# Kernel tuning notes

Measured on AMD Instinct MI355X. Metric: run time of the kernel, lower is better.

## Reference

```python
import jax, jax.numpy as jnp
import numpy as np

B, S, D = 4, 2048, 512
H, DH = 8, 64          # heads, dim_head; inner_dim = H*DH = D
QN, QP = -128, 127     # signed 8-bit range (LSQ, all_positive=False)
UQP = 255              # unsigned 8-bit range for softmax output

# scale-vector layout (one learnable LSQ scale per quantizer, as in the module)
# 0:s_hs 1:s_a_q 2:s_w_q 3:s_a_k 4:s_w_k 5:s_a_v 6:s_w_v
# 7:s_qk_a 8:s_qk_b 9:s_softmax 10:s_av_a 11:s_av_b 12:s_a_out 13:s_w_out

def fq(x, s, qn=QN, qp=QP):
    """LSQ fake quantization: clamp(round(x/s), qn, qp) * s, STE on round."""
    v = jnp.clip(x / s, qn, qp)
    vq = v + jax.lax.stop_gradient(jnp.round(v) - v)
    return vq * s


def setup_inputs() -> dict:
    key = jax.random.key(0)
    ks = jax.random.split(key, 6)
    hs = jax.random.normal(ks[0], (B, S, D), dtype=jnp.float32)
    w_std = 0.02
    Wq = jax.random.normal(ks[1], (D, D), dtype=jnp.float32) * w_std
    Wk = jax.random.normal(ks[2], (D, D), dtype=jnp.float32) * w_std
    Wv = jax.random.normal(ks[3], (D, D), dtype=jnp.float32) * w_std
    Wo = jax.random.normal(ks[4], (D, D), dtype=jnp.float32) * w_std
    bo = jnp.zeros((D,), dtype=jnp.float32)
    scales = jnp.array([
        0.03,    # s_hs: hs ~ N(0,1), clip at ~4 sigma
        0.03, 0.001,   # to_q act / weight
        0.03, 0.001,   # to_k act / weight
        0.03, 0.001,   # to_v act / weight
        0.02, 0.02,    # mul_qk a/b
        1.0 / 255.0,   # softmax output (unsigned)
        1.0 / 255.0, 0.02,  # mul_av a/b
        0.01, 0.001,   # to_out act / weight
    ], dtype=jnp.float32)
    return {"hs": hs, "Wq": Wq, "Wk": Wk, "Wv": Wv, "Wo": Wo, "bo": bo,
            "scales": scales}


def reference(hs, Wq, Wk, Wv, Wo, bo, scales):
    sc = scales
    scale = DH ** (-0.5)
    # quan_hs_before_attn (encoder_hidden_states = hs in self-attention)
    hs_q = fq(hs, sc[0])
    # Linear_Quan: LSQ-quantized activation @ LSQ-quantized weight
    def qlin(x, W, sa, sw):
        return jnp.einsum('bsd,ed->bse', fq(x, sa), fq(W, sw))
    q = qlin(hs_q, Wq, sc[1], sc[2])
    k = qlin(hs_q, Wk, sc[3], sc[4])
    v = qlin(hs_q, Wv, sc[5], sc[6])
    # 'b s (h d) -> b h s d'
    q = q.reshape(B, S, H, DH).transpose(0, 2, 1, 3)
    k = k.reshape(B, S, H, DH).transpose(0, 2, 1, 3)
    v = v.reshape(B, S, H, DH).transpose(0, 2, 1, 3)
    # QuanMMHead(q, k^T): quantize both operands, then matmul
    attn = jnp.einsum('bhsd,bhtd->bhst', fq(q, sc[7]), fq(k, sc[8])) * scale
    # QuanSoftmax: softmax then unsigned 8-bit fake quant of probabilities
    attn = fq(jax.nn.softmax(attn, axis=-1), sc[9], 0, UQP)
    # QuanMMHead(attn, v)
    out = jnp.einsum('bhst,bhtd->bhsd', fq(attn, sc[10]), fq(v, sc[11]))
    # '(b h) s d -> b s (h d)'
    out = out.transpose(0, 2, 1, 3).reshape(B, S, H * DH)
    # to_out[0]: Linear_Quan with bias (dropout is identity in eval)
    out = jnp.einsum('bsd,ed->bse', fq(out, sc[12]), fq(Wo, sc[13])) + bo
    return out
```

## Files before the change

### kernel.cpp

```cpp
#include <hip/hip_runtime.h>

typedef _Float16 half8  __attribute__((ext_vector_type(8)));
typedef float    f32x4  __attribute__((ext_vector_type(4)));
typedef int      i32x4  __attribute__((ext_vector_type(4)));
typedef unsigned short ushort8 __attribute__((ext_vector_type(8)));
typedef signed char char8 __attribute__((ext_vector_type(8)));

__device__ __forceinline__ float clampf(float v, float lo, float hi){
    return fminf(fmaxf(v, lo), hi);
}
__device__ __forceinline__ float b2f(unsigned short u){
    unsigned int x = ((unsigned int)u) << 16;
    return __builtin_bit_cast(float, x);
}
__device__ __forceinline__ unsigned short f2b(float f){
    unsigned int u = __builtin_bit_cast(unsigned int, f);
    u += 0x7FFFu + ((u >> 16) & 1u);
    return (unsigned short)(u >> 16);
}
__device__ __forceinline__ float fexp2(float x){ return __builtin_amdgcn_exp2f(x); }

__device__ __forceinline__ void gld_lds16(const void* g, void* lds_uniform){
    __builtin_amdgcn_global_load_lds(
        (const __attribute__((address_space(1))) void*)g,
        (__attribute__((address_space(3))) void*)lds_uniform, 16, 0, 0);
}

#define BW_WALL 0u
#define BW_WO   786432u
#define BW_AQ   1048576u
#define BW_AK   (BW_AQ + 4194304u)
#define BW_AV   (BW_AK + 4194304u)
#define BW_Q    (BW_AV + 4194304u)
#define BW_K    (BW_Q  + 8388608u)
#define BW_VT   (BW_K  + 8388608u)
#define BW_O    (BW_VT + 8388608u)

__global__ __launch_bounds__(256) void k_quant(
    const unsigned short* __restrict__ hs,
    const unsigned short* __restrict__ Wq, const unsigned short* __restrict__ Wk,
    const unsigned short* __restrict__ Wv, const unsigned short* __restrict__ Wo,
    signed char* __restrict__ w_all, signed char* __restrict__ wo8,
    signed char* __restrict__ aq, signed char* __restrict__ ak,
    signed char* __restrict__ av,
    const unsigned short* __restrict__ scu)
{
    int blk = blockIdx.x;
    if (blk < 512){
        int gid  = blk * 256 + threadIdx.x;
        int idx8 = gid * 8;
        int which = idx8 >> 18;
        int rem   = idx8 & 262143;
        const unsigned short* W = (which==0)? Wq : (which==1)? Wk : (which==2)? Wv : Wo;
        float sw = b2f((which<3) ? scu[2 + 2*which] : scu[13]);
        ushort8 w = *(const ushort8*)(W + rem);
        char8 o;
        #pragma unroll
        for (int j=0;j<8;j++)
            o[j] = (signed char)rintf(clampf(b2f(w[j])/sw, -128.f, 127.f));
        signed char* dst = (which<3) ? (w_all + which*262144 + rem) : (wo8 + rem);
        *(char8*)dst = o;
    } else {
        int gid = (blk - 512) * 256 + threadIdx.x;
        int i8 = gid * 8;
        float s0 = b2f(scu[0]), s1 = b2f(scu[1]), s3 = b2f(scu[3]), s5 = b2f(scu[5]);
        ushort8 h = *(const ushort8*)(hs + i8);
        char8 q, k, v;
        #pragma unroll
        for (int j=0;j<8;j++){
            float h1 = rintf(clampf(b2f(h[j])/s0, -128.f, 127.f)) * s0;
            q[j] = (signed char)rintf(clampf(h1/s1, -128.f, 127.f));
            k[j] = (signed char)rintf(clampf(h1/s3, -128.f, 127.f));
            v[j] = (signed char)rintf(clampf(h1/s5, -128.f, 127.f));
        }
        *(char8*)(aq+i8) = q;
        *(char8*)(ak+i8) = k;
        *(char8*)(av+i8) = v;
    }
}

__global__ __launch_bounds__(256) void k_gemm_qkv(
    const signed char* __restrict__ aq, const signed char* __restrict__ ak,
    const signed char* __restrict__ av, const signed char* __restrict__ w_all,
    _Float16* __restrict__ q16, _Float16* __restrict__ k16, _Float16* __restrict__ vt16,
    const unsigned short* __restrict__ scu)
{
    __shared__ __align__(16) union SMem {
        struct { signed char At[128][64]; signed char Bt[64][64]; } ab;
        _Float16 Vt[64][132];
    } sm;
    int tid = threadIdx.x;
    int m0 = blockIdx.x*128, n0 = blockIdx.y*64;
    int proj = blockIdx.y >> 3;
    const signed char* Ag = (proj==0)? aq : (proj==1)? ak : av;
    int w = tid>>6, lane = tid&63, l15 = lane&15, quad = lane>>4;
    int wm = w>>1, wn = w&1;
    i32x4 z = {0,0,0,0};
    i32x4 acc[4][2];
    #pragma unroll
    for (int i=0;i<4;i++)
      #pragma unroll
      for (int j=0;j<2;j++) acc[i][j] = z;

    for (int k0=0; k0<512; k0+=64){
        #pragma unroll
        for (int it=0; it<2; it++){
            int idx = it*256 + tid;
            int row = idx>>2, col = (idx&3)*16;
            int ubase = (it*256 + w*64)*16;
            gld_lds16(Ag + (m0+row)*512 + k0 + col, &sm.ab.At[0][0] + ubase);
        }
        {
            int row = tid>>2, col = (tid&3)*16;
            int ubase = (w*64)*16;
            gld_lds16(w_all + (n0+row)*512 + k0 + col, &sm.ab.Bt[0][0] + ubase);
        }
        __syncthreads();
        i32x4 af[4], bf[2];
        #pragma unroll
        for (int mt=0; mt<4; mt++)
            af[mt] = *(const i32x4*)(&sm.ab.At[wm*64+mt*16+l15][quad*16]);
        #pragma unroll
        for (int nt=0; nt<2; nt++)
            bf[nt] = *(const i32x4*)(&sm.ab.Bt[wn*32+nt*16+l15][quad*16]);
        #pragma unroll
        for (int mt=0; mt<4; mt++)
          #pragma unroll
          for (int nt=0; nt<2; nt++)
            acc[mt][nt] = __builtin_amdgcn_mfma_i32_16x16x64_i8(af[mt], bf[nt], acc[mt][nt], 0,0,0);
        __syncthreads();
    }

    float ssc = b2f(scu[1+2*proj]) * b2f(scu[2+2*proj]);
    float qs  = b2f((proj==0)? scu[7] : (proj==1)? scu[8] : scu[11]);
    if (proj < 2){
        #pragma unroll
        for (int mt=0; mt<4; mt++){
          #pragma unroll
          for (int nt=0; nt<2; nt++){
            int n = n0 + wn*32 + nt*16 + l15;
            int nloc = n & 511;
            int h = nloc>>6, d = nloc&63;
            #pragma unroll
            for (int r=0;r<4;r++){
              int m = m0 + wm*64 + mt*16 + quad*4 + r;
              int b = m>>11, s = m&2047;
              int bh = b*8 + h;
              float val = (float)acc[mt][nt][r] * ssc;
              float qv = rintf(clampf(val/qs, -128.f, 127.f));
              if (proj==0) q16[(bh*2048 + s)*64 + d] = (_Float16)qv;
              else         k16[(bh*2048 + s)*64 + d] = (_Float16)qv;
            }
          }
        }
    } else {
        #pragma unroll
        for (int mt=0; mt<4; mt++){
          #pragma unroll
          for (int nt=0; nt<2; nt++){
            int nl = wn*32 + nt*16 + l15;
            #pragma unroll
            for (int r=0;r<4;r++){
              int ml = wm*64 + mt*16 + quad*4 + r;
              float val = (float)acc[mt][nt][r] * ssc;
              sm.Vt[nl][ml] = (_Float16)rintf(clampf(val/qs, -128.f, 127.f));
            }
          }
        }
        __syncthreads();
        int vrow = tid >> 2;
        int vcol = (tid & 3) * 32;
        int nloc2 = (n0 & 511) + vrow;
        int h2 = nloc2 >> 6, d2 = nloc2 & 63;
        int bh2 = (m0 >> 11)*8 + h2;
        int s2 = (m0 & 2047) + vcol;
        _Float16* dst = vt16 + (bh2*64 + d2)*2048 + s2;
        #pragma unroll
        for (int i=0;i<4;i++)
            *(half8*)(dst + i*8) = *(const half8*)(&sm.Vt[vrow][vcol + i*8]);
    }
}

__global__ __launch_bounds__(512, 4) void k_attn(
    const _Float16* __restrict__ q16, const _Float16* __restrict__ k16,
    const _Float16* __restrict__ vt16, signed char* __restrict__ o8,
    const unsigned short* __restrict__ scu)
{
    __shared__ __align__(16) _Float16 Kbuf[2][64][72];
    __shared__ __align__(16) _Float16 p16[8][16][72];
    int tid = threadIdx.x;
    int w = tid>>6, lane = tid&63, l15 = lane&15, quad = lane>>4;
    int bh = blockIdx.x;
    int q0 = blockIdx.y*128 + w*16;
    float s9 = b2f(scu[9]), s10 = b2f(scu[10]);
    float al2 = b2f(scu[7]) * b2f(scu[8]) * 0.125f * 1.44269504088896341f;

    f32x4 z = {0.f,0.f,0.f,0.f};
    const _Float16* qr = q16 + (bh*2048 + q0 + l15)*64;
    half8 aq0 = *(const half8*)(qr + quad*8);
    half8 aq1 = *(const half8*)(qr + 32 + quad*8);

    const _Float16* kg    = k16  + bh*131072;
    const _Float16* vbase = vt16 + bh*131072;
    int srow = tid>>3, scol = (tid&7)*8;

    half8 kst = *(const half8*)(kg + tid*8);

    float l[4] = {0.f, 0.f, 0.f, 0.f};
    float cmx[32];

    #pragma unroll
    for (int ch=0; ch<32; ch++){
        int buf = ch & 1;
        *(half8*)(&Kbuf[buf][srow][scol]) = kst;
        __syncthreads();
        if (ch < 31)
            kst = *(const half8*)(kg + (ch+1)*4096 + tid*8);
        f32x4 s[4];
        #pragma unroll
        for (int j=0;j<4;j++){
            half8 bk0 = *(const half8*)(&Kbuf[buf][j*16+l15][quad*8]);
            half8 bk1 = *(const half8*)(&Kbuf[buf][j*16+l15][32+quad*8]);
            f32x4 t = __builtin_amdgcn_mfma_f32_16x16x32_f16(aq0, bk0, z, 0,0,0);
            s[j]    = __builtin_amdgcn_mfma_f32_16x16x32_f16(aq1, bk1, t, 0,0,0);
        }
        float mj[4];
        #pragma unroll
        for (int j=0;j<4;j++){
            mj[j] = fmaxf(fmaxf(s[j][0], s[j][1]), fmaxf(s[j][2], s[j][3]));
            #pragma unroll
            for (int r=0;r<4;r++)
                l[r] += fexp2(s[j][r]*al2);
        }
        cmx[ch] = fmaxf(fmaxf(mj[0], mj[1]), fmaxf(mj[2], mj[3]));
    }

    #pragma unroll
    for (int r=0;r<4;r++){
        #pragma unroll
        for (int d=1; d<16; d<<=1)
            l[r] += __shfl_xor(l[r], d, 64);
    }
    float inv_s9 = 1.0f / s9;
    float r910   = s9 / s10;
    float lq9[4];
    #pragma unroll
    for (int r=0;r<4;r++) lq9[r] = log2f(inv_s9 / l[r]);
    float lml = fmaxf(fmaxf(lq9[0], lq9[1]), fmaxf(lq9[2], lq9[3]));
    unsigned int mask = 0u;
    #pragma unroll
    for (int ch=0; ch<32; ch++){
        if (__ballot(fmaf(cmx[ch], al2, lml) > -1.0001f)) mask |= (1u << ch);
    }

    f32x4 oacc[4];
    #pragma unroll
    for (int dt=0; dt<4; dt++) oacc[dt] = z;
    for (int ch=0; ch<32; ch++){
        if (!(mask & (1u << ch))) continue;
        const _Float16* kc = kg + ch*4096;
        f32x4 s[4];
        #pragma unroll
        for (int j=0;j<4;j++){
            const _Float16* kr = kc + (j*16+l15)*64;
            half8 bk0 = *(const half8*)(kr + quad*8);
            half8 bk1 = *(const half8*)(kr + 32 + quad*8);
            f32x4 t = __builtin_amdgcn_mfma_f32_16x16x32_f16(aq0, bk0, z, 0,0,0);
            s[j]    = __builtin_amdgcn_mfma_f32_16x16x32_f16(aq1, bk1, t, 0,0,0);
        }
        float rmax[4];
        #pragma unroll
        for (int r=0;r<4;r++)
            rmax[r] = fmaxf(fmaxf(s[0][r], s[1][r]), fmaxf(s[2][r], s[3][r]));
        float rb = fmaxf(fmaxf(fmaf(rmax[0], al2, lq9[0]), fmaf(rmax[1], al2, lq9[1])),
                         fmaxf(fmaf(rmax[2], al2, lq9[2]), fmaf(rmax[3], al2, lq9[3])));
        if (!__ballot(rb > -1.0001f)) continue;

        float av[4][4];
        float amax = 0.f;
        #pragma unroll
        for (int j=0;j<4;j++){
            #pragma unroll
            for (int r=0;r<4;r++){
                float p1i = rintf(fminf(fexp2(fmaf(s[j][r], al2, lq9[r])), 255.f));
                float a   = rintf(fminf(p1i*r910, 127.f));
                av[j][r] = a;
                amax = fmaxf(amax, a);
            }
        }
        if (__ballot(amax > 0.f)){
            #pragma unroll
            for (int j=0;j<4;j++)
                #pragma unroll
                for (int r=0;r<4;r++)
                    p16[w][quad*4+r][j*16+l15] = (_Float16)av[j][r];
            half8 ap0 = *(const half8*)(&p16[w][l15][quad*8]);
            half8 ap1 = *(const half8*)(&p16[w][l15][32+quad*8]);
            #pragma unroll
            for (int dt=0; dt<4; dt++){
                const _Float16* vr0 = vbase + (dt*16+l15)*2048 + ch*64;
                half8 b0 = *(const half8*)(vr0 + quad*8);
                half8 b1 = *(const half8*)(vr0 + 32 + quad*8);
                oacc[dt] = __builtin_amdgcn_mfma_f32_16x16x32_f16(ap0, b0, oacc[dt], 0,0,0);
                oacc[dt] = __builtin_amdgcn_mfma_f32_16x16x32_f16(ap1, b1, oacc[dt], 0,0,0);
            }
        }
    }

    float s1011 = b2f(scu[10]) * b2f(scu[11]);
    float s12   = b2f(scu[12]);
    int b = bh>>3, h = bh&7;
    #pragma unroll
    for (int dt=0; dt<4; dt++){
        #pragma unroll
        for (int r=0;r<4;r++){
            float o = oacc[dt][r] * s1011;
            signed char v = (signed char)rintf(clampf(o/s12, -128.f, 127.f));
            o8[(b*2048 + q0 + quad*4 + r)*512 + h*64 + dt*16 + l15] = v;
        }
    }
}

__global__ __launch_bounds__(256) void k_gemm_out(
    const signed char* __restrict__ o8, const signed char* __restrict__ wo8,
    const unsigned short* __restrict__ bo, unsigned short* __restrict__ out,
    const unsigned short* __restrict__ scu)
{
    __shared__ __align__(16) signed char At[64][64];
    __shared__ __align__(16) signed char Bt[64][64];
    int tid = threadIdx.x;
    int m0 = blockIdx.x*64, n0 = blockIdx.y*64;
    int w = tid>>6, lane = tid&63, l15 = lane&15, quad = lane>>4;
    int wm = w>>1, wn = w&1;
    i32x4 z = {0,0,0,0};
    i32x4 acc[2][2];
    #pragma unroll
    for (int i=0;i<2;i++)
      #pragma unroll
      for (int j=0;j<2;j++) acc[i][j] = z;

    for (int k0=0; k0<512; k0+=64){
        {
            int row = tid>>2, col = (tid&3)*16;
            int ubase = (w*64)*16;
            gld_lds16(o8  + (m0+row)*512 + k0 + col, &At[0][0] + ubase);
        }
        {
            int row = tid>>2, col = (tid&3)*16;
            int ubase = (w*64)*16;
            gld_lds16(wo8 + (n0+row)*512 + k0 + col, &Bt[0][0] + ubase);
        }
        __syncthreads();
        i32x4 af[2], bf[2];
        #pragma unroll
        for (int mt=0; mt<2; mt++)
            af[mt] = *(const i32x4*)(&At[wm*32+mt*16+l15][quad*16]);
        #pragma unroll
        for (int nt=0; nt<2; nt++)
            bf[nt] = *(const i32x4*)(&Bt[wn*32+nt*16+l15][quad*16]);
        #pragma unroll
        for (int mt=0; mt<2; mt++)
          #pragma unroll
          for (int nt=0; nt<2; nt++)
            acc[mt][nt] = __builtin_amdgcn_mfma_i32_16x16x64_i8(af[mt], bf[nt], acc[mt][nt], 0,0,0);
        __syncthreads();
    }

    float ssc = b2f(scu[12]) * b2f(scu[13]);
    #pragma unroll
    for (int mt=0; mt<2; mt++){
      #pragma unroll
      for (int nt=0; nt<2; nt++){
        int n = n0 + wn*32 + nt*16 + l15;
        float bn = b2f(bo[n]);
        #pragma unroll
        for (int r=0;r<4;r++){
          int m = m0 + wm*32 + mt*16 + quad*4 + r;
          out[m*512 + n] = f2b((float)acc[mt][nt][r]*ssc + bn);
        }
      }
    }
}

extern "C" void kernel_launch(void* const* d_in, const int* in_sizes, int n_in,
                              void* d_out, int out_size, void* d_ws, size_t ws_size,
                              hipStream_t stream)
{
    const unsigned short* hs = (const unsigned short*)d_in[0];
    const unsigned short* Wq = (const unsigned short*)d_in[1];
    const unsigned short* Wk = (const unsigned short*)d_in[2];
    const unsigned short* Wv = (const unsigned short*)d_in[3];
    const unsigned short* Wo = (const unsigned short*)d_in[4];
    const unsigned short* bo = (const unsigned short*)d_in[5];
    const unsigned short* sc = (const unsigned short*)d_in[6];
    unsigned short* out = (unsigned short*)d_out;

    unsigned char* ws = (unsigned char*)d_ws;
    signed char* w_all = (signed char*)(ws + BW_WALL);
    signed char* wo8   = (signed char*)(ws + BW_WO);
    signed char* a_q   = (signed char*)(ws + BW_AQ);
    signed char* a_k   = (signed char*)(ws + BW_AK);
    signed char* a_v   = (signed char*)(ws + BW_AV);
    _Float16*    q16   = (_Float16*)(ws + BW_Q);
    _Float16*    k16   = (_Float16*)(ws + BW_K);
    _Float16*    vt16  = (_Float16*)(ws + BW_VT);
    signed char* o8    = (signed char*)(ws + BW_O);

    k_quant<<<2560, 256, 0, stream>>>(hs, Wq, Wk, Wv, Wo, w_all, wo8,
                                      a_q, a_k, a_v, sc);
    k_gemm_qkv<<<dim3(64,24), 256, 0, stream>>>(a_q, a_k, a_v, w_all, q16, k16, vt16, sc);
    k_attn<<<dim3(32,16), 512, 0, stream>>>(q16, k16, vt16, o8, sc);
    k_gemm_out<<<dim3(128,8), 256, 0, stream>>>(o8, wo8, bo, out, sc);
}
```

Baseline: 144.5 us.

## Store Q/K/V as int8 and run attention matmuls with int8 MFMA

Quantized Q, K and V^T were held as fp16 integer values. They are now stored as int8, and both attention matmuls (QK^T and PV) use the i32 16x16x64 int8 MFMA in place of pairs of f16 16x16x32 MFMAs. This halves the memory traffic and LDS footprint for Q/K/V and halves the MFMA instruction count. It also requires int-to-float conversions of the scores, and the LDS padding is changed to suit byte-wide rows.

```diff
diff --git a/kernel.cpp b/kernel.cpp
--- a/kernel.cpp
+++ b/kernel.cpp
@@ -32,9 +32,9 @@
 #define BW_AK   (BW_AQ + 4194304u)
 #define BW_AV   (BW_AK + 4194304u)
 #define BW_Q    (BW_AV + 4194304u)
-#define BW_K    (BW_Q  + 8388608u)
-#define BW_VT   (BW_K  + 8388608u)
-#define BW_O    (BW_VT + 8388608u)
+#define BW_K    (BW_Q  + 4194304u)
+#define BW_VT   (BW_K  + 4194304u)
+#define BW_O    (BW_VT + 4194304u)
 
 __global__ __launch_bounds__(256) void k_quant(
     const unsigned short* __restrict__ hs,
@@ -82,12 +82,13 @@
 __global__ __launch_bounds__(256) void k_gemm_qkv(
     const signed char* __restrict__ aq, const signed char* __restrict__ ak,
     const signed char* __restrict__ av, const signed char* __restrict__ w_all,
-    _Float16* __restrict__ q16, _Float16* __restrict__ k16, _Float16* __restrict__ vt16,
+    signed char* __restrict__ q8, signed char* __restrict__ k8,
+    signed char* __restrict__ vt8,
     const unsigned short* __restrict__ scu)
 {
     __shared__ __align__(16) union SMem {
         struct { signed char At[128][64]; signed char Bt[64][64]; } ab;
-        _Float16 Vt[64][132];
+        signed char Vt[64][144];
     } sm;
     int tid = threadIdx.x;
     int m0 = blockIdx.x*128, n0 = blockIdx.y*64;
@@ -147,9 +148,9 @@
               int b = m>>11, s = m&2047;
               int bh = b*8 + h;
               float val = (float)acc[mt][nt][r] * ssc;
-              float qv = rintf(clampf(val/qs, -128.f, 127.f));
-              if (proj==0) q16[(bh*2048 + s)*64 + d] = (_Float16)qv;
-              else         k16[(bh*2048 + s)*64 + d] = (_Float16)qv;
+              signed char qv = (signed char)rintf(clampf(val/qs, -128.f, 127.f));
+              if (proj==0) q8[(bh*2048 + s)*64 + d] = qv;
+              else         k8[(bh*2048 + s)*64 + d] = qv;
             }
           }
         }
@@ -163,7 +164,7 @@
             for (int r=0;r<4;r++){
               int ml = wm*64 + mt*16 + quad*4 + r;
               float val = (float)acc[mt][nt][r] * ssc;
-              sm.Vt[nl][ml] = (_Float16)rintf(clampf(val/qs, -128.f, 127.f));
+              sm.Vt[nl][ml] = (signed char)rintf(clampf(val/qs, -128.f, 127.f));
             }
           }
         }
@@ -174,20 +175,19 @@
         int h2 = nloc2 >> 6, d2 = nloc2 & 63;
         int bh2 = (m0 >> 11)*8 + h2;
         int s2 = (m0 & 2047) + vcol;
-        _Float16* dst = vt16 + (bh2*64 + d2)*2048 + s2;
-        #pragma unroll
-        for (int i=0;i<4;i++)
-            *(half8*)(dst + i*8) = *(const half8*)(&sm.Vt[vrow][vcol + i*8]);
+        signed char* dst = vt8 + (bh2*64 + d2)*2048 + s2;
+        *(i32x4*)(dst)      = *(const i32x4*)(&sm.Vt[vrow][vcol]);
+        *(i32x4*)(dst + 16) = *(const i32x4*)(&sm.Vt[vrow][vcol + 16]);
     }
 }
 
 __global__ __launch_bounds__(512, 4) void k_attn(
-    const _Float16* __restrict__ q16, const _Float16* __restrict__ k16,
-    const _Float16* __restrict__ vt16, signed char* __restrict__ o8,
+    const signed char* __restrict__ q8, const signed char* __restrict__ k8,
+    const signed char* __restrict__ vt8, signed char* __restrict__ o8,
     const unsigned short* __restrict__ scu)
 {
-    __shared__ __align__(16) _Float16 Kbuf[2][64][72];
-    __shared__ __align__(16) _Float16 p16[8][16][72];
+    __shared__ __align__(16) signed char Kbuf[2][64][80];
+    __shared__ __align__(16) signed char p8s[8][16][80];
     int tid = threadIdx.x;
     int w = tid>>6, lane = tid&63, l15 = lane&15, quad = lane>>4;
     int bh = blockIdx.x;
@@ -195,16 +195,15 @@
     float s9 = b2f(scu[9]), s10 = b2f(scu[10]);
     float al2 = b2f(scu[7]) * b2f(scu[8]) * 0.125f * 1.44269504088896341f;
 
-    f32x4 z = {0.f,0.f,0.f,0.f};
-    const _Float16* qr = q16 + (bh*2048 + q0 + l15)*64;
-    half8 aq0 = *(const half8*)(qr + quad*8);
-    half8 aq1 = *(const half8*)(qr + 32 + quad*8);
-
-    const _Float16* kg    = k16  + bh*131072;
-    const _Float16* vbase = vt16 + bh*131072;
+    i32x4 zi = {0,0,0,0};
+    const signed char* qr = q8 + (bh*2048 + q0 + l15)*64;
+    i32x4 aqf = *(const i32x4*)(qr + quad*16);
+
+    const signed char* kg    = k8  + bh*131072;
+    const signed char* vbase = vt8 + bh*131072;
     int srow = tid>>3, scol = (tid&7)*8;
 
-    half8 kst = *(const half8*)(kg + tid*8);
+    char8 kst = *(const char8*)(kg + tid*8);
 
     float l[4] = {0.f, 0.f, 0.f, 0.f};
     float cmx[32];
@@ -212,17 +211,17 @@
     #pragma unroll
     for (int ch=0; ch<32; ch++){
         int buf = ch & 1;
-        *(half8*)(&Kbuf[buf][srow][scol]) = kst;
+        *(char8*)(&Kbuf[buf][srow][scol]) = kst;
         __syncthreads();
         if (ch < 31)
-            kst = *(const half8*)(kg + (ch+1)*4096 + tid*8);
-        f32x4 s[4];
+            kst = *(const char8*)(kg + (ch+1)*4096 + tid*8);
+        float s[4][4];
         #pragma unroll
         for (int j=0;j<4;j++){
-            half8 bk0 = *(const half8*)(&Kbuf[buf][j*16+l15][quad*8]);
-            half8 bk1 = *(const half8*)(&Kbuf[buf][j*16+l15][32+quad*8]);
-            f32x4 t = __builtin_amdgcn_mfma_f32_16x16x32_f16(aq0, bk0, z, 0,0,0);
-            s[j]    = __builtin_amdgcn_mfma_f32_16x16x32_f16(aq1, bk1, t, 0,0,0);
+            i32x4 bk = *(const i32x4*)(&Kbuf[buf][j*16+l15][quad*16]);
+            i32x4 si = __builtin_amdgcn_mfma_i32_16x16x64_i8(aqf, bk, zi, 0,0,0);
+            #pragma unroll
+            for (int r=0;r<4;r++) s[j][r] = (float)si[r];
         }
         float mj[4];
         #pragma unroll
@@ -253,20 +252,20 @@
         if (__ballot(fmaf(cmx[ch], al2, lml) > -1.0001f)) mask |= (1u << ch);
     }
 
-    f32x4 oacc[4];
-    #pragma unroll
-    for (int dt=0; dt<4; dt++) oacc[dt] = z;
+    i32x4 oacc[4];
+    #pragma unroll
+    for (int dt=0; dt<4; dt++) oacc[dt] = zi;
     for (int ch=0; ch<32; ch++){
         if (!(mask & (1u << ch))) continue;
-        const _Float16* kc = kg + ch*4096;
-        f32x4 s[4];
+        const signed char* kc = kg + ch*4096;
+        float s[4][4];
         #pragma unroll
         for (int j=0;j<4;j++){
-            const _Float16* kr = kc + (j*16+l15)*64;
-            half8 bk0 = *(const half8*)(kr + quad*8);
-            half8 bk1 = *(const half8*)(kr + 32 + quad*8);
-            f32x4 t = __builtin_amdgcn_mfma_f32_16x16x32_f16(aq0, bk0, z, 0,0,0);
-            s[j]    = __builtin_amdgcn_mfma_f32_16x16x32_f16(aq1, bk1, t, 0,0,0);
+            const signed char* kr = kc + (j*16+l15)*64;
+            i32x4 bk = *(const i32x4*)(kr + quad*16);
+            i32x4 si = __builtin_amdgcn_mfma_i32_16x16x64_i8(aqf, bk, zi, 0,0,0);
+            #pragma unroll
+            for (int r=0;r<4;r++) s[j][r] = (float)si[r];
         }
         float rmax[4];
         #pragma unroll
@@ -293,16 +292,13 @@
             for (int j=0;j<4;j++)
                 #pragma unroll
                 for (int r=0;r<4;r++)
-                    p16[w][quad*4+r][j*16+l15] = (_Float16)av[j][r];
-            half8 ap0 = *(const half8*)(&p16[w][l15][quad*8]);
-            half8 ap1 = *(const half8*)(&p16[w][l15][32+quad*8]);
+                    p8s[w][quad*4+r][j*16+l15] = (signed char)av[j][r];
+            i32x4 ap = *(const i32x4*)(&p8s[w][l15][quad*16]);
             #pragma unroll
             for (int dt=0; dt<4; dt++){
-                const _Float16* vr0 = vbase + (dt*16+l15)*2048 + ch*64;
-                half8 b0 = *(const half8*)(vr0 + quad*8);
-                half8 b1 = *(const half8*)(vr0 + 32 + quad*8);
-                oacc[dt] = __builtin_amdgcn_mfma_f32_16x16x32_f16(ap0, b0, oacc[dt], 0,0,0);
-                oacc[dt] = __builtin_amdgcn_mfma_f32_16x16x32_f16(ap1, b1, oacc[dt], 0,0,0);
+                const signed char* vr0 = vbase + (dt*16+l15)*2048 + ch*64;
+                i32x4 bv = *(const i32x4*)(vr0 + quad*16);
+                oacc[dt] = __builtin_amdgcn_mfma_i32_16x16x64_i8(ap, bv, oacc[dt], 0,0,0);
             }
         }
     }
@@ -314,7 +310,7 @@
     for (int dt=0; dt<4; dt++){
         #pragma unroll
         for (int r=0;r<4;r++){
-            float o = oacc[dt][r] * s1011;
+            float o = (float)oacc[dt][r] * s1011;
             signed char v = (signed char)rintf(clampf(o/s12, -128.f, 127.f));
             o8[(b*2048 + q0 + quad*4 + r)*512 + h*64 + dt*16 + l15] = v;
         }
@@ -401,14 +397,14 @@
     signed char* a_q   = (signed char*)(ws + BW_AQ);
     signed char* a_k   = (signed char*)(ws + BW_AK);
     signed char* a_v   = (signed char*)(ws + BW_AV);
-    _Float16*    q16   = (_Float16*)(ws + BW_Q);
-    _Float16*    k16   = (_Float16*)(ws + BW_K);
-    _Float16*    vt16  = (_Float16*)(ws + BW_VT);
+    signed char* q8    = (signed char*)(ws + BW_Q);
+    signed char* k8    = (signed char*)(ws + BW_K);
+    signed char* vt8   = (signed char*)(ws + BW_VT);
     signed char* o8    = (signed char*)(ws + BW_O);
 
     k_quant<<<2560, 256, 0, stream>>>(hs, Wq, Wk, Wv, Wo, w_all, wo8,
                                       a_q, a_k, a_v, sc);
-    k_gemm_qkv<<<dim3(64,24), 256, 0, stream>>>(a_q, a_k, a_v, w_all, q16, k16, vt16, sc);
-    k_attn<<<dim3(32,16), 512, 0, stream>>>(q16, k16, vt16, o8, sc);
+    k_gemm_qkv<<<dim3(64,24), 256, 0, stream>>>(a_q, a_k, a_v, w_all, q8, k8, vt8, sc);
+    k_attn<<<dim3(32,16), 512, 0, stream>>>(q8, k8, vt8, o8, sc);
     k_gemm_out<<<dim3(128,8), 256, 0, stream>>>(o8, wo8, bo, out, sc);
 }
```

Result: no change. 141.7 us (-1.9%).
